# Kernel tuning notes

Measured on AMD Instinct MI355X. Metric: run time of the kernel, lower is better.

The kernel has to match this reference:

```python
import jax, jax.numpy as jnp
import numpy as np

N, E, IN_DIM, HID, OUT = 50000, 600000, 128, 256, 128

def setup_inputs() -> dict:
    key = jax.random.key(0)
    k1, k2, k3, k4, k5, k6, k7 = jax.random.split(key, 7)
    h = jax.random.normal(k1, (N, IN_DIM), dtype=jnp.float32)
    src = jax.random.randint(k2, (E,), 0, N)
    dst = jax.random.randint(k3, (E,), 0, N)
    s1 = 1.0 / np.sqrt(2 * IN_DIM)
    s2 = 1.0 / np.sqrt(HID)
    W1 = jax.random.uniform(k4, (2 * IN_DIM, HID), minval=-s1, maxval=s1, dtype=jnp.float32)
    b1 = jax.random.uniform(k5, (HID,), minval=-s1, maxval=s1, dtype=jnp.float32)
    W2 = jax.random.uniform(k6, (HID, OUT), minval=-s2, maxval=s2, dtype=jnp.float32)
    b2 = jax.random.uniform(k7, (OUT,), minval=-s2, maxval=s2, dtype=jnp.float32)
    return {"h": h, "src": src, "dst": dst, "W1": W1, "b1": b1, "W2": W2, "b2": b2}

def reference(h, src, dst, W1, b1, W2, b2):
    n = h.shape[0]
    # copy_u + mean: gather src features, segment-sum at dst, divide by in-degree
    msg_sum = jax.ops.segment_sum(h[src], dst, num_segments=n)          # [N, D]
    deg = jax.ops.segment_sum(jnp.ones((src.shape[0],), h.dtype), dst, num_segments=n)
    h_neigh = msg_sum / jnp.maximum(deg, 1.0)[:, None]                  # zero-deg nodes -> 0
    h_total = jnp.concatenate([h, h_neigh], axis=1)                     # [N, 2D]
    out = (h_total @ W1 + b1) @ W2 + b2                                 # 2-layer MLP (no inner activation)
    return jax.nn.relu(out)
```

## Files before the change

### kernel.cpp

```cpp
#include <hip/hip_runtime.h>

#define N_NODES 50000
#define E_EDGES 600000
#define IN_DIM  128
#define HID     256
#define OUT_DIM 128
#define CAP     64

#define RANGE_N 6250
#define CHUNK_E 2048
#define NB_FILL 2344
#define NB_HCVT 3125
#define NB_WCVT 384
#define NB_PREP (NB_FILL + NB_HCVT + NB_WCVT)
#define NB_MLP  782

typedef __bf16 bf16x8 __attribute__((ext_vector_type(8)));
typedef float  f32x16 __attribute__((ext_vector_type(16)));
typedef unsigned short ushort8 __attribute__((ext_vector_type(8)));

__device__ __forceinline__ unsigned short f2bf(float f) {
    union { float f; unsigned int i; } v; v.f = f;
    unsigned int b = v.i;
    b += 0x7fffu + ((b >> 16) & 1u);
    return (unsigned short)(b >> 16);
}
__device__ __forceinline__ void acc2(unsigned u, float& a0, float& a1) {
    union { unsigned i; float f; } lo, hi;
    lo.i = u << 16; hi.i = u & 0xffff0000u;
    a0 += lo.f; a1 += hi.f;
}

__global__ void __launch_bounds__(256)
sage_prep(const int* __restrict__ src, const int* __restrict__ dst,
          int* __restrict__ counts, char* __restrict__ outb,
          const float* __restrict__ h, unsigned short* __restrict__ ht,
          const float* __restrict__ W1, const float* __restrict__ W2,
          unsigned short* __restrict__ w1sw, unsigned short* __restrict__ w2sw) {
    int b = blockIdx.x;
    if (b < NB_FILL) {
        int r = b & 7;
        int chunk = b >> 3;
        int e0 = chunk * CHUNK_E + threadIdx.x * 8;
        if (e0 < E_EDGES) {
            int lo = r * RANGE_N, hi = lo + RANGE_N;
            const int4 d0 = *(const int4*)(dst + e0);
            const int4 d1 = *(const int4*)(dst + e0 + 4);
            int dd[8] = {d0.x, d0.y, d0.z, d0.w, d1.x, d1.y, d1.z, d1.w};
            #pragma unroll
            for (int k = 0; k < 8; ++k) {
                int d = dd[k];
                if (d >= lo && d < hi) {
                    int s = src[e0 + k];
                    int sl = atomicAdd(counts + d, 1);
                    if (sl < CAP) *((int*)(outb + (size_t)d * 512 + 256) + sl) = s;
                }
            }
        }
    } else if (b < NB_FILL + NB_HCVT) {
        int idx = (b - NB_FILL) * 256 + threadIdx.x;
        int n = idx >> 4, g = idx & 15;
        const float4 v0 = *(const float4*)(h + (size_t)n * IN_DIM + g * 8);
        const float4 v1 = *(const float4*)(h + (size_t)n * IN_DIM + g * 8 + 4);
        ushort8 o;
        o[0] = f2bf(v0.x); o[1] = f2bf(v0.y); o[2] = f2bf(v0.z); o[3] = f2bf(v0.w);
        o[4] = f2bf(v1.x); o[5] = f2bf(v1.y); o[6] = f2bf(v1.z); o[7] = f2bf(v1.w);
        *(ushort8*)(ht + (size_t)n * 128 + g * 8) = o;
    } else {
        int i1 = (b - NB_FILL - NB_HCVT) * 256 + threadIdx.x;
        if (i1 < 65536) {
            int j = i1 & 7, n = (i1 >> 3) & 255, g = (i1 >> 11) & 1, ks = (i1 >> 12) & 3, c = i1 >> 14;
            int k = c * 64 + ks * 16 + g * 8 + j;
            w1sw[i1] = f2bf(W1[(size_t)k * HID + n]);
        } else {
            int i2 = i1 - 65536;
            int j = i2 & 7, n = (i2 >> 3) & 127, g = (i2 >> 10) & 1, ks = (i2 >> 11) & 7, c = (i2 >> 14) & 1;
            int k = c * 128 + ks * 16 + g * 8 + j;
            w2sw[i2] = f2bf(W2[(size_t)k * OUT_DIM + n]);
        }
    }
}

__global__ void __launch_bounds__(256, 4)
sage_fused(const int* __restrict__ counts,
           const unsigned short* __restrict__ ht,
           const unsigned short* __restrict__ w1sw,
           const unsigned short* __restrict__ w2sw,
           const float* __restrict__ b1,
           const float* __restrict__ b2,
           float* out) {
    __shared__ unsigned short hid_s[64][264];

    const int t = threadIdx.x;
    const int nw = t >> 6;
    const int lane = t & 63;
    const int lr = lane & 31;
    const int lg = lane >> 5;
    const int base = blockIdx.x * 64;
    const int row0 = min(base + lr,      N_NODES - 1);
    const int row1 = min(base + 32 + lr, N_NODES - 1);

    {
        #pragma unroll 1
        for (int i = 0; i < 16; ++i) {
            int m = nw * 16 + i;
            int node = min(base + m, N_NODES - 1);
            int dg = counts[node];
            int entries = min(dg, CAP);
            const int* bk = (const int*)((const char*)out + (size_t)node * 512 + 256);
            float a0 = 0.f, a1 = 0.f;
            int e = 0;
            for (; e + 8 <= entries; e += 8) {
                const int4 q0 = *(const int4*)(bk + e);
                const int4 q1 = *(const int4*)(bk + e + 4);
                unsigned u0 = *(const unsigned*)(ht + (size_t)q0.x * 128 + lane * 2);
                unsigned u1 = *(const unsigned*)(ht + (size_t)q0.y * 128 + lane * 2);
                unsigned u2 = *(const unsigned*)(ht + (size_t)q0.z * 128 + lane * 2);
                unsigned u3 = *(const unsigned*)(ht + (size_t)q0.w * 128 + lane * 2);
                unsigned u4 = *(const unsigned*)(ht + (size_t)q1.x * 128 + lane * 2);
                unsigned u5 = *(const unsigned*)(ht + (size_t)q1.y * 128 + lane * 2);
                unsigned u6 = *(const unsigned*)(ht + (size_t)q1.z * 128 + lane * 2);
                unsigned u7 = *(const unsigned*)(ht + (size_t)q1.w * 128 + lane * 2);
                acc2(u0, a0, a1); acc2(u1, a0, a1); acc2(u2, a0, a1); acc2(u3, a0, a1);
                acc2(u4, a0, a1); acc2(u5, a0, a1); acc2(u6, a0, a1); acc2(u7, a0, a1);
            }
            if (e + 4 <= entries) {
                const int4 q = *(const int4*)(bk + e);
                unsigned u0 = *(const unsigned*)(ht + (size_t)q.x * 128 + lane * 2);
                unsigned u1 = *(const unsigned*)(ht + (size_t)q.y * 128 + lane * 2);
                unsigned u2 = *(const unsigned*)(ht + (size_t)q.z * 128 + lane * 2);
                unsigned u3 = *(const unsigned*)(ht + (size_t)q.w * 128 + lane * 2);
                acc2(u0, a0, a1); acc2(u1, a0, a1); acc2(u2, a0, a1); acc2(u3, a0, a1);
                e += 4;
            }
            for (; e < entries; ++e) {
                unsigned u = *(const unsigned*)(ht + (size_t)bk[e] * 128 + lane * 2);
                acc2(u, a0, a1);
            }
            float inv = 1.0f / (float)max(dg, 1);
            unsigned o = (unsigned)f2bf(a0 * inv) | ((unsigned)f2bf(a1 * inv) << 16);
            *(unsigned*)(&hid_s[m][lane * 2]) = o;
        }
    }

    f32x16 c1[2][2];
    #pragma unroll
    for (int e2 = 0; e2 < 16; ++e2) {
        c1[0][0][e2] = 0.f; c1[0][1][e2] = 0.f; c1[1][0][e2] = 0.f; c1[1][1][e2] = 0.f;
    }

    #pragma unroll
    for (int c = 0; c < 2; ++c) {
        bf16x8 a0[4], a1[4];
        #pragma unroll
        for (int ks = 0; ks < 4; ++ks) {
            int koff = (c * 4 + ks) * 16 + lg * 8;
            a0[ks] = *(const bf16x8*)(ht + (size_t)row0 * 128 + koff);
            a1[ks] = *(const bf16x8*)(ht + (size_t)row1 * 128 + koff);
        }
        #pragma unroll
        for (int ks = 0; ks < 4; ++ks) {
            #pragma unroll
            for (int nt = 0; nt < 2; ++nt) {
                int n = nw * 64 + nt * 32 + lr;
                bf16x8 b = *(const bf16x8*)(w1sw + c * 16384 + (((ks * 2 + lg) * 256) + n) * 8);
                c1[0][nt] = __builtin_amdgcn_mfma_f32_32x32x16_bf16(a0[ks], b, c1[0][nt], 0, 0, 0);
                c1[1][nt] = __builtin_amdgcn_mfma_f32_32x32x16_bf16(a1[ks], b, c1[1][nt], 0, 0, 0);
            }
        }
    }

    __syncthreads();

    #pragma unroll
    for (int c = 2; c < 4; ++c) {
        bf16x8 a0[4], a1[4];
        #pragma unroll
        for (int ks = 0; ks < 4; ++ks) {
            int koff = (c - 2) * 64 + ks * 16 + lg * 8;
            a0[ks] = *(const bf16x8*)(&hid_s[lr][koff]);
            a1[ks] = *(const bf16x8*)(&hid_s[32 + lr][koff]);
        }
        #pragma unroll
        for (int ks = 0; ks < 4; ++ks) {
            #pragma unroll
            for (int nt = 0; nt < 2; ++nt) {
                int n = nw * 64 + nt * 32 + lr;
                bf16x8 b = *(const bf16x8*)(w1sw + c * 16384 + (((ks * 2 + lg) * 256) + n) * 8);
                c1[0][nt] = __builtin_amdgcn_mfma_f32_32x32x16_bf16(a0[ks], b, c1[0][nt], 0, 0, 0);
                c1[1][nt] = __builtin_amdgcn_mfma_f32_32x32x16_bf16(a1[ks], b, c1[1][nt], 0, 0, 0);
            }
        }
    }

    __syncthreads();

    #pragma unroll
    for (int nt = 0; nt < 2; ++nt) {
        int col = nw * 64 + nt * 32 + lr;
        float bias = b1[col];
        #pragma unroll
        for (int s = 0; s < 2; ++s) {
            #pragma unroll
            for (int reg = 0; reg < 16; ++reg) {
                int m = s * 32 + (reg & 3) + 8 * (reg >> 2) + 4 * lg;
                hid_s[m][col] = f2bf(c1[s][nt][reg] + bias);
            }
        }
    }
    __syncthreads();

    f32x16 c2[2];
    #pragma unroll
    for (int e2 = 0; e2 < 16; ++e2) { c2[0][e2] = 0.f; c2[1][e2] = 0.f; }

    #pragma unroll
    for (int c = 0; c < 2; ++c) {
        #pragma unroll
        for (int ks = 0; ks < 8; ++ks) {
            bf16x8 b = *(const bf16x8*)(w2sw + c * 16384 + ((ks * 2 + lg) * 128 + nw * 32 + lr) * 8);
            int koff = c * 128 + ks * 16 + lg * 8;
            bf16x8 ah0 = *(const bf16x8*)(&hid_s[lr][koff]);
            bf16x8 ah1 = *(const bf16x8*)(&hid_s[32 + lr][koff]);
            c2[0] = __builtin_amdgcn_mfma_f32_32x32x16_bf16(ah0, b, c2[0], 0, 0, 0);
            c2[1] = __builtin_amdgcn_mfma_f32_32x32x16_bf16(ah1, b, c2[1], 0, 0, 0);
        }
    }

    {
        int col = nw * 32 + lr;
        float bias = b2[col];
        #pragma unroll
        for (int s = 0; s < 2; ++s) {
            #pragma unroll
            for (int reg = 0; reg < 16; ++reg) {
                int m = s * 32 + (reg & 3) + 8 * (reg >> 2) + 4 * lg;
                int n = base + m;
                if (n < N_NODES)
                    out[(size_t)n * OUT_DIM + col] = fmaxf(c2[s][reg] + bias, 0.0f);
            }
        }
    }
}

extern "C" void kernel_launch(void* const* d_in, const int* in_sizes, int n_in,
                              void* d_out, int out_size, void* d_ws, size_t ws_size,
                              hipStream_t stream) {
    const float* h   = (const float*)d_in[0];
    const int*   src = (const int*)d_in[1];
    const int*   dst = (const int*)d_in[2];
    const float* W1  = (const float*)d_in[3];
    const float* b1  = (const float*)d_in[4];
    const float* W2  = (const float*)d_in[5];
    const float* b2  = (const float*)d_in[6];
    float* out = (float*)d_out;

    int* counts = (int*)d_ws;
    unsigned short* w1sw = (unsigned short*)(counts + N_NODES);
    unsigned short* w2sw = w1sw + 65536;
    unsigned short* ht   = w2sw + 32768;

    hipMemsetAsync(counts, 0, N_NODES * sizeof(int), stream);

    sage_prep<<<NB_PREP, 256, 0, stream>>>(
        src, dst, counts, (char*)d_out, h, ht, W1, W2, w1sw, w2sw);

    sage_fused<<<NB_MLP, 256, 0, stream>>>(counts, ht, w1sw, w2sw, b1, b2, out);
}
```

Before: 184.7 us.

## Interleave neighbor gathers across four nodes and split prep kernel into fill and convert

The aggregation loop now processes four destination nodes at once per wave, prefetching the next four neighbor indices per node and issuing up to sixteen independent row gathers before accumulating. This aims to raise memory-level parallelism in the latency-bound gather. Degree and index values are made wave-uniform with readfirstlane. The combined prep kernel is split into separate fill and convert kernels, which adds a launch but removes divergent block-role dispatch. The padded per-node loop costs some predicated iterations when degrees differ.

```diff
diff --git a/kernel.cpp b/kernel.cpp
--- a/kernel.cpp
+++ b/kernel.cpp
@@ -12,7 +12,7 @@
 #define NB_FILL 2344
 #define NB_HCVT 3125
 #define NB_WCVT 384
-#define NB_PREP (NB_FILL + NB_HCVT + NB_WCVT)
+#define NB_CVT  (NB_HCVT + NB_WCVT)
 #define NB_MLP  782
 
 typedef __bf16 bf16x8 __attribute__((ext_vector_type(8)));
@@ -32,33 +32,36 @@
 }
 
 __global__ void __launch_bounds__(256)
-sage_prep(const int* __restrict__ src, const int* __restrict__ dst,
-          int* __restrict__ counts, char* __restrict__ outb,
-          const float* __restrict__ h, unsigned short* __restrict__ ht,
-          const float* __restrict__ W1, const float* __restrict__ W2,
-          unsigned short* __restrict__ w1sw, unsigned short* __restrict__ w2sw) {
+sage_fill(const int* __restrict__ src, const int* __restrict__ dst,
+          int* __restrict__ counts, char* __restrict__ outb) {
     int b = blockIdx.x;
-    if (b < NB_FILL) {
-        int r = b & 7;
-        int chunk = b >> 3;
-        int e0 = chunk * CHUNK_E + threadIdx.x * 8;
-        if (e0 < E_EDGES) {
-            int lo = r * RANGE_N, hi = lo + RANGE_N;
-            const int4 d0 = *(const int4*)(dst + e0);
-            const int4 d1 = *(const int4*)(dst + e0 + 4);
-            int dd[8] = {d0.x, d0.y, d0.z, d0.w, d1.x, d1.y, d1.z, d1.w};
-            #pragma unroll
-            for (int k = 0; k < 8; ++k) {
-                int d = dd[k];
-                if (d >= lo && d < hi) {
-                    int s = src[e0 + k];
-                    int sl = atomicAdd(counts + d, 1);
-                    if (sl < CAP) *((int*)(outb + (size_t)d * 512 + 256) + sl) = s;
-                }
-            }
-        }
-    } else if (b < NB_FILL + NB_HCVT) {
-        int idx = (b - NB_FILL) * 256 + threadIdx.x;
+    int r = b & 7;
+    int chunk = b >> 3;
+    int e0 = chunk * CHUNK_E + threadIdx.x * 8;
+    if (e0 < E_EDGES) {
+        int lo = r * RANGE_N, hi = lo + RANGE_N;
+        const int4 d0 = *(const int4*)(dst + e0);
+        const int4 d1 = *(const int4*)(dst + e0 + 4);
+        int dd[8] = {d0.x, d0.y, d0.z, d0.w, d1.x, d1.y, d1.z, d1.w};
+        #pragma unroll
+        for (int k = 0; k < 8; ++k) {
+            int d = dd[k];
+            if (d >= lo && d < hi) {
+                int s = src[e0 + k];
+                int sl = atomicAdd(counts + d, 1);
+                if (sl < CAP) *((int*)(outb + (size_t)d * 512 + 256) + sl) = s;
+            }
+        }
+    }
+}
+
+__global__ void __launch_bounds__(256)
+sage_cvt(const float* __restrict__ h, unsigned short* __restrict__ ht,
+         const float* __restrict__ W1, const float* __restrict__ W2,
+         unsigned short* __restrict__ w1sw, unsigned short* __restrict__ w2sw) {
+    int b = blockIdx.x;
+    if (b < NB_HCVT) {
+        int idx = b * 256 + threadIdx.x;
         int n = idx >> 4, g = idx & 15;
         const float4 v0 = *(const float4*)(h + (size_t)n * IN_DIM + g * 8);
         const float4 v1 = *(const float4*)(h + (size_t)n * IN_DIM + g * 8 + 4);
@@ -67,7 +70,7 @@
         o[4] = f2bf(v1.x); o[5] = f2bf(v1.y); o[6] = f2bf(v1.z); o[7] = f2bf(v1.w);
         *(ushort8*)(ht + (size_t)n * 128 + g * 8) = o;
     } else {
-        int i1 = (b - NB_FILL - NB_HCVT) * 256 + threadIdx.x;
+        int i1 = (b - NB_HCVT) * 256 + threadIdx.x;
         if (i1 < 65536) {
             int j = i1 & 7, n = (i1 >> 3) & 255, g = (i1 >> 11) & 1, ks = (i1 >> 12) & 3, c = i1 >> 14;
             int k = c * 64 + ks * 16 + g * 8 + j;
@@ -102,44 +105,59 @@
 
     {
         #pragma unroll 1
-        for (int i = 0; i < 16; ++i) {
-            int m = nw * 16 + i;
-            int node = min(base + m, N_NODES - 1);
-            int dg = counts[node];
-            int entries = min(dg, CAP);
-            const int* bk = (const int*)((const char*)out + (size_t)node * 512 + 256);
-            float a0 = 0.f, a1 = 0.f;
-            int e = 0;
-            for (; e + 8 <= entries; e += 8) {
-                const int4 q0 = *(const int4*)(bk + e);
-                const int4 q1 = *(const int4*)(bk + e + 4);
-                unsigned u0 = *(const unsigned*)(ht + (size_t)q0.x * 128 + lane * 2);
-                unsigned u1 = *(const unsigned*)(ht + (size_t)q0.y * 128 + lane * 2);
-                unsigned u2 = *(const unsigned*)(ht + (size_t)q0.z * 128 + lane * 2);
-                unsigned u3 = *(const unsigned*)(ht + (size_t)q0.w * 128 + lane * 2);
-                unsigned u4 = *(const unsigned*)(ht + (size_t)q1.x * 128 + lane * 2);
-                unsigned u5 = *(const unsigned*)(ht + (size_t)q1.y * 128 + lane * 2);
-                unsigned u6 = *(const unsigned*)(ht + (size_t)q1.z * 128 + lane * 2);
-                unsigned u7 = *(const unsigned*)(ht + (size_t)q1.w * 128 + lane * 2);
-                acc2(u0, a0, a1); acc2(u1, a0, a1); acc2(u2, a0, a1); acc2(u3, a0, a1);
-                acc2(u4, a0, a1); acc2(u5, a0, a1); acc2(u6, a0, a1); acc2(u7, a0, a1);
-            }
-            if (e + 4 <= entries) {
-                const int4 q = *(const int4*)(bk + e);
-                unsigned u0 = *(const unsigned*)(ht + (size_t)q.x * 128 + lane * 2);
-                unsigned u1 = *(const unsigned*)(ht + (size_t)q.y * 128 + lane * 2);
-                unsigned u2 = *(const unsigned*)(ht + (size_t)q.z * 128 + lane * 2);
-                unsigned u3 = *(const unsigned*)(ht + (size_t)q.w * 128 + lane * 2);
-                acc2(u0, a0, a1); acc2(u1, a0, a1); acc2(u2, a0, a1); acc2(u3, a0, a1);
-                e += 4;
-            }
-            for (; e < entries; ++e) {
-                unsigned u = *(const unsigned*)(ht + (size_t)bk[e] * 128 + lane * 2);
-                acc2(u, a0, a1);
-            }
-            float inv = 1.0f / (float)max(dg, 1);
-            unsigned o = (unsigned)f2bf(a0 * inv) | ((unsigned)f2bf(a1 * inv) << 16);
-            *(unsigned*)(&hid_s[m][lane * 2]) = o;
+        for (int g = 0; g < 4; ++g) {
+            const int m0 = nw * 16 + g * 4;
+            float a0[4], a1[4];
+            int deg[4], ent[4];
+            const int* bk[4];
+            int4 q[4];
+            int em = 0;
+            #pragma unroll
+            for (int j = 0; j < 4; ++j) {
+                a0[j] = 0.f; a1[j] = 0.f;
+                int node = min(base + m0 + j, N_NODES - 1);
+                deg[j] = __builtin_amdgcn_readfirstlane(counts[node]);
+                ent[j] = min(deg[j], CAP);
+                em = max(em, ent[j]);
+                bk[j] = (const int*)((const char*)out + (size_t)node * 512 + 256);
+                q[j] = *(const int4*)(bk[j]);
+            }
+            #pragma unroll 1
+            for (int p = 0; p < em; p += 4) {
+                int4 nx[4];
+                #pragma unroll
+                for (int j = 0; j < 4; ++j)
+                    nx[j] = *(const int4*)(bk[j] + min(p + 4, CAP - 4));
+                unsigned uu[16];
+                #pragma unroll
+                for (int k = 0; k < 4; ++k) {
+                    #pragma unroll
+                    for (int j = 0; j < 4; ++j) {
+                        if (p + k < ent[j]) {
+                            int idx = (k == 0) ? q[j].x : (k == 1) ? q[j].y
+                                    : (k == 2) ? q[j].z : q[j].w;
+                            idx = __builtin_amdgcn_readfirstlane(idx);
+                            uu[k * 4 + j] = *(const unsigned*)(ht + (size_t)idx * 128 + lane * 2);
+                        }
+                    }
+                }
+                #pragma unroll
+                for (int k = 0; k < 4; ++k) {
+                    #pragma unroll
+                    for (int j = 0; j < 4; ++j) {
+                        if (p + k < ent[j])
+                            acc2(uu[k * 4 + j], a0[j], a1[j]);
+                    }
+                }
+                #pragma unroll
+                for (int j = 0; j < 4; ++j) q[j] = nx[j];
+            }
+            #pragma unroll
+            for (int j = 0; j < 4; ++j) {
+                float inv = 1.0f / (float)max(deg[j], 1);
+                unsigned o = (unsigned)f2bf(a0[j] * inv) | ((unsigned)f2bf(a1[j] * inv) << 16);
+                *(unsigned*)(&hid_s[m0 + j][lane * 2]) = o;
+            }
         }
     }
 
@@ -262,8 +280,9 @@
 
     hipMemsetAsync(counts, 0, N_NODES * sizeof(int), stream);
 
-    sage_prep<<<NB_PREP, 256, 0, stream>>>(
-        src, dst, counts, (char*)d_out, h, ht, W1, W2, w1sw, w2sw);
+    sage_fill<<<NB_FILL, 256, 0, stream>>>(src, dst, counts, (char*)d_out);
+
+    sage_cvt<<<NB_CVT, 256, 0, stream>>>(h, ht, W1, W2, w1sw, w2sw);
 
     sage_fused<<<NB_MLP, 256, 0, stream>>>(counts, ht, w1sw, w2sw, b1, b2, out);
 }
```

Result: faster. 177.7 us (-3.8%).
